# Kernel optimization log

Hardware: AMD Instinct MI355X
Metric: run time of the kernel (lower is better)

Reference implementation:

```python
import math
import jax, jax.numpy as jnp
import numpy as np

H_HEADS = 8
K_MAX = 64
MIN_WINDOW = 1.0
SHARPNESS = 5.0


def rmsnorm(x, w, eps=1e-6):
    x32 = x.astype(jnp.float32)
    var = jnp.mean(x32 * x32, axis=-1, keepdims=True)
    return (w * (x32 * jax.lax.rsqrt(var + eps))).astype(x.dtype)


def setup_inputs() -> dict:
    key = jax.random.key(0)
    ks = jax.random.split(key, 12)
    B, L, C = 1, 4096, 256
    H, K = H_HEADS, K_MAX
    s = 0.02
    return {
        "x": jax.random.normal(ks[0], (B, L, C), jnp.float32),
        "window_w": jax.random.normal(ks[1], (C, H), jnp.float32) * s,
        "window_b": jnp.zeros((H,), jnp.float32),
        "window_gamma": jnp.ones((H,), jnp.float32),
        "offset_w": jax.random.normal(ks[2], (C, H), jnp.float32) * s,
        "offset_b": jnp.zeros((H,), jnp.float32),
        "offset_gamma": jnp.ones((H,), jnp.float32),
        "kernel_w": jax.random.normal(ks[3], (C, H * K), jnp.float32) * s,
        "kernel_b": jnp.zeros((H * K,), jnp.float32),
        "kernel_gamma": jnp.ones((H * K,), jnp.float32),
        "v_w": jax.random.normal(ks[4], (C, C), jnp.float32) * (1.0 / math.sqrt(C)),
        "v_b": jnp.zeros((C,), jnp.float32),
        "out_w": jax.random.normal(ks[5], (C, C), jnp.float32) * s,
    }


def reference(x, window_w, window_b, window_gamma, offset_w, offset_b, offset_gamma,
              kernel_w, kernel_b, kernel_gamma, v_w, v_b, out_w):
    B, L, C = x.shape
    H, K = H_HEADS, K_MAX
    D = C // H
    max_window = min(int(math.sqrt(L)), K)
    half = max_window // 2
    max_offset = int(math.sqrt(L))
    N = 2 * half + 1  # num_offsets

    # per-position learned window sizes, center offsets, kernel weights
    window_raw = jax.nn.sigmoid(rmsnorm(x @ window_w + window_b, window_gamma))
    window_sizes = MIN_WINDOW + window_raw * (max_window - MIN_WINDOW)      # [B,L,H]
    center_offsets = jnp.tanh(rmsnorm(x @ offset_w + offset_b, offset_gamma)) * max_offset  # [B,L,H]
    kernel_weights = jax.nn.silu(rmsnorm(x @ kernel_w + kernel_b, kernel_gamma)).reshape(B, L, H, K)
    v = (x @ v_w + v_b).reshape(B, L, H, D)

    local = jnp.arange(-half, half + 1, dtype=x.dtype)                      # [N]
    positions = jnp.arange(L, dtype=x.dtype).reshape(1, L, 1, 1)
    neighbor = positions + center_offsets[..., None] + local.reshape(1, 1, 1, N)  # [B,L,H,N]
    valid = (neighbor >= 0) & (neighbor < L)
    nclamp = jnp.clip(neighbor, 0, L - 1)

    rel = jnp.abs(local).reshape(1, 1, 1, N) / (window_sizes[..., None] / 2 + 1e-6)
    window_mask = jax.nn.sigmoid(SHARPNESS * (1.0 - rel)) * valid.astype(x.dtype)

    # kernel interpolation by relative distance
    kidx = jnp.clip(rel, 0, 1) * (K - 1)
    i_fl = jnp.clip(kidx.astype(jnp.int32), 0, K - 2)                       # [B,L,H,N]
    i_ce = i_fl + 1
    w_ce = kidx - i_fl.astype(x.dtype)
    k_fl = jnp.take_along_axis(kernel_weights, i_fl, axis=-1)
    k_ce = jnp.take_along_axis(kernel_weights, i_ce, axis=-1)
    kernel_interp = k_fl * (1.0 - w_ce) + k_ce * w_ce

    attn = kernel_interp * window_mask
    attn = attn / (jnp.sum(attn, axis=-1, keepdims=True) + 1e-6)            # [B,L,H,N]

    # bilinear gather of values at fractional neighbor positions
    p_fl = jnp.clip(jnp.floor(nclamp).astype(jnp.int32), 0, L - 1)
    p_ce = jnp.clip(p_fl + 1, 0, L - 1)
    frac = nclamp - p_fl.astype(x.dtype)                                    # [B,L,H,N]

    v_bh = v.transpose(0, 2, 1, 3)                                          # [B,H,L,D]
    idx_f = p_fl.transpose(0, 2, 1, 3).reshape(B, H, L * N)
    idx_c = p_ce.transpose(0, 2, 1, 3).reshape(B, H, L * N)
    v_fl = jnp.take_along_axis(v_bh, idx_f[..., None], axis=2).reshape(B, H, L, N, D)
    v_ce = jnp.take_along_axis(v_bh, idx_c[..., None], axis=2).reshape(B, H, L, N, D)
    frac_bh = frac.transpose(0, 2, 1, 3)[..., None]                         # [B,H,L,N,1]
    v_nb = v_fl * (1.0 - frac_bh) + v_ce * frac_bh                          # [B,H,L,N,D]

    attn_bh = attn.transpose(0, 2, 1, 3)                                    # [B,H,L,N]
    out = jnp.einsum('bhln,bhlnd->bhld', attn_bh, v_nb)                     # [B,H,L,D]
    out = out.transpose(0, 2, 1, 3).reshape(B, L, C)
    return jax.nn.silu(out @ out_w)
```

## Files before the change

### kernel.cpp

```cpp
#include <hip/hip_runtime.h>
#include <math.h>

#define L_SEQ 4096
#define C_DIM 256
#define H_HEADS 8
#define K_MAX 64
#define D_HEAD 32
#define HALF_W 32
#define N_OFF 65
#define HK 512

__device__ __forceinline__ float sigmoidf_(float x) { return 1.0f / (1.0f + expf(-x)); }

__global__ void __launch_bounds__(128, 2)
proj_gemm(const float* __restrict__ A, const float* __restrict__ kw_w,
          const float* __restrict__ vw, const float* __restrict__ kb,
          const float* __restrict__ vb,
          float* __restrict__ kwbuf, float* __restrict__ vbuf) {
    __shared__ float As[16][132];
    __shared__ float Bs[16][68];

    const int tid = threadIdx.x;
    const int tx = tid & 7;
    const int ty = tid >> 3;
    const int l0 = blockIdx.y * 128;
    const int n0 = blockIdx.x * 64;

    const int arow = tid;
    const int bk = tid >> 3;
    const int bn = (tid & 7) * 8;

    const float* Bsrc;
    int ldb, coff;
    if (n0 < 512) { Bsrc = kw_w; ldb = 512; coff = n0; }
    else          { Bsrc = vw;   ldb = 256; coff = n0 - 512; }

    float acc[8][8];
#pragma unroll
    for (int i = 0; i < 8; ++i)
#pragma unroll
        for (int jj = 0; jj < 8; ++jj) acc[i][jj] = 0.0f;

    const float* arow_p = A + (l0 + arow) * C_DIM;
    float4 a0 = *(const float4*)&arow_p[0];
    float4 a1 = *(const float4*)&arow_p[4];
    float4 a2 = *(const float4*)&arow_p[8];
    float4 a3 = *(const float4*)&arow_p[12];
    float4 b0 = *(const float4*)&Bsrc[bk * ldb + coff + bn];
    float4 b1 = *(const float4*)&Bsrc[bk * ldb + coff + bn + 4];

    for (int k0 = 0; k0 < C_DIM; k0 += 16) {
        __syncthreads();
        As[0][arow]  = a0.x; As[1][arow]  = a0.y; As[2][arow]  = a0.z; As[3][arow]  = a0.w;
        As[4][arow]  = a1.x; As[5][arow]  = a1.y; As[6][arow]  = a1.z; As[7][arow]  = a1.w;
        As[8][arow]  = a2.x; As[9][arow]  = a2.y; As[10][arow] = a2.z; As[11][arow] = a2.w;
        As[12][arow] = a3.x; As[13][arow] = a3.y; As[14][arow] = a3.z; As[15][arow] = a3.w;
        *(float4*)&Bs[bk][bn]     = b0;
        *(float4*)&Bs[bk][bn + 4] = b1;
        __syncthreads();
        if (k0 + 16 < C_DIM) {
            a0 = *(const float4*)&arow_p[k0 + 16 + 0];
            a1 = *(const float4*)&arow_p[k0 + 16 + 4];
            a2 = *(const float4*)&arow_p[k0 + 16 + 8];
            a3 = *(const float4*)&arow_p[k0 + 16 + 12];
            b0 = *(const float4*)&Bsrc[(k0 + 16 + bk) * ldb + coff + bn];
            b1 = *(const float4*)&Bsrc[(k0 + 16 + bk) * ldb + coff + bn + 4];
        }
#pragma unroll
        for (int kk = 0; kk < 16; ++kk) {
            const float4 alo = *(const float4*)&As[kk][ty * 8];
            const float4 ahi = *(const float4*)&As[kk][ty * 8 + 4];
            const float4 blo = *(const float4*)&Bs[kk][tx * 8];
            const float4 bhi = *(const float4*)&Bs[kk][tx * 8 + 4];
            const float ar[8] = {alo.x, alo.y, alo.z, alo.w, ahi.x, ahi.y, ahi.z, ahi.w};
            const float br[8] = {blo.x, blo.y, blo.z, blo.w, bhi.x, bhi.y, bhi.z, bhi.w};
#pragma unroll
            for (int i = 0; i < 8; ++i)
#pragma unroll
                for (int jj = 0; jj < 8; ++jj)
                    acc[i][jj] = fmaf(ar[i], br[jj], acc[i][jj]);
        }
    }

    const int g0 = n0 + tx * 8;
    float4 bz0, bz1;
    float* dst;
    int stride, col;
    if (g0 < 512) {
        bz0 = *(const float4*)&kb[g0]; bz1 = *(const float4*)&kb[g0 + 4];
        dst = kwbuf; stride = 512; col = g0;
    } else {
        bz0 = *(const float4*)&vb[g0 - 512]; bz1 = *(const float4*)&vb[g0 - 508];
        dst = vbuf; stride = 256; col = g0 - 512;
    }
#pragma unroll
    for (int i = 0; i < 8; ++i) {
        const int row = l0 + ty * 8 + i;
        float4 o0, o1;
        o0.x = acc[i][0] + bz0.x; o0.y = acc[i][1] + bz0.y;
        o0.z = acc[i][2] + bz0.z; o0.w = acc[i][3] + bz0.w;
        o1.x = acc[i][4] + bz1.x; o1.y = acc[i][5] + bz1.y;
        o1.z = acc[i][6] + bz1.z; o1.w = acc[i][7] + bz1.w;
        *(float4*)&dst[row * stride + col]     = o0;
        *(float4*)&dst[row * stride + col + 4] = o1;
    }
}

__global__ void __launch_bounds__(512, 1)
conv_fused(const float* __restrict__ x,
           const float* __restrict__ ww, const float* __restrict__ wb,
           const float* __restrict__ wg,
           const float* __restrict__ ow, const float* __restrict__ ob,
           const float* __restrict__ og,
           const float* __restrict__ kg,
           const float* __restrict__ kwraw, const float* __restrict__ v,
           float* __restrict__ out) {
    const int l = blockIdx.x;
    const int tid = threadIdx.x;

    __shared__ float red[256];
    __shared__ float rs_s;
    __shared__ float kwrow[HK];
    __shared__ float wsz[H_HEADS], ofs[H_HEADS];
    __shared__ float4 tap[H_HEADS][N_OFF];
    __shared__ float2 warr[H_HEADS][N_OFF + 1];
    __shared__ float inv_denom[H_HEADS];
    __shared__ int okflag;

    float z0 = 0.0f, z1 = 0.0f;
    if (tid < 256) {
        const float* row = kwraw + l * HK;
        z0 = row[tid];
        z1 = row[tid + 256];
        red[tid] = z0 * z0 + z1 * z1;
    } else if (tid < 320) {
        const int lane = tid - 256;
        const float* xr = x + l * C_DIM;
        float accw[H_HEADS], acco[H_HEADS];
#pragma unroll
        for (int h = 0; h < H_HEADS; ++h) { accw[h] = 0.0f; acco[h] = 0.0f; }
#pragma unroll
        for (int i = 0; i < C_DIM / 64; ++i) {
            const int c = lane + i * 64;
            const float xv = xr[c];
            const float* wwc = ww + c * H_HEADS;
            const float* owc = ow + c * H_HEADS;
#pragma unroll
            for (int h = 0; h < H_HEADS; ++h) {
                accw[h] = fmaf(xv, wwc[h], accw[h]);
                acco[h] = fmaf(xv, owc[h], acco[h]);
            }
        }
#pragma unroll
        for (int off = 32; off > 0; off >>= 1) {
#pragma unroll
            for (int h = 0; h < H_HEADS; ++h) {
                accw[h] += __shfl_xor(accw[h], off);
                acco[h] += __shfl_xor(acco[h], off);
            }
        }
        if (lane < H_HEADS) {
            float zw[H_HEADS], zo[H_HEADS];
            float ssw = 0.0f, sso = 0.0f;
#pragma unroll
            for (int h = 0; h < H_HEADS; ++h) {
                zw[h] = accw[h] + wb[h];
                zo[h] = acco[h] + ob[h];
                ssw += zw[h] * zw[h];
                sso += zo[h] * zo[h];
            }
            const float rw = rsqrtf(ssw / (float)H_HEADS + 1e-6f);
            const float ro = rsqrtf(sso / (float)H_HEADS + 1e-6f);
            const float nw = wg[lane] * zw[lane] * rw;
            const float no = og[lane] * zo[lane] * ro;
            wsz[lane] = 1.0f + sigmoidf_(nw) * 63.0f;
            ofs[lane] = tanhf(no) * 64.0f;
        }
    }
    if (tid == 0) okflag = 1;
    __syncthreads();

    if (tid < 128) red[tid] += red[tid + 128];
    __syncthreads();
    if (tid < 64) {
        red[tid] += red[tid + 64];
        if (tid < 32) red[tid] += red[tid + 32];
        if (tid < 16) red[tid] += red[tid + 16];
        if (tid < 8)  red[tid] += red[tid + 8];
        if (tid < 4)  red[tid] += red[tid + 4];
        if (tid < 2)  red[tid] += red[tid + 2];
        if (tid < 1) {
            red[0] += red[1];
            rs_s = rsqrtf(red[0] / (float)HK + 1e-6f);
        }
    }
    __syncthreads();
    if (tid < 256) {
        const float rs = rs_s;
        const float n0v = kg[tid] * z0 * rs;
        const float n1v = kg[tid + 256] * z1 * rs;
        kwrow[tid]       = n0v * sigmoidf_(n0v);
        kwrow[tid + 256] = n1v * sigmoidf_(n1v);
    }
    __syncthreads();

    for (int t = tid; t < H_HEADS * N_OFF; t += 512) {
        const int h = t / N_OFF;
        const int n = t - h * N_OFF;
        const float ws  = wsz[h];
        const float off = ofs[h];
        const float local = (float)(n - HALF_W);
        const float neighbor = (float)l + off + local;
        const bool valid = (neighbor >= 0.0f) && (neighbor < (float)L_SEQ);
        const float nc = fminf(fmaxf(neighbor, 0.0f), (float)(L_SEQ - 1));

        const float rel = fabsf(local) / (ws * 0.5f + 1e-6f);
        const float mask = sigmoidf_(5.0f * (1.0f - rel)) * (valid ? 1.0f : 0.0f);

        const float kidx = fminf(rel, 1.0f) * (float)(K_MAX - 1);
        int ifl = (int)kidx;
        ifl = min(ifl, K_MAX - 2);
        const float wce = kidx - (float)ifl;
        const float kf = kwrow[h * K_MAX + ifl];
        const float kc = kwrow[h * K_MAX + ifl + 1];
        const float attnv = (kf * (1.0f - wce) + kc * wce) * mask;

        int p = (int)floorf(nc);
        p = min(max(p, 0), L_SEQ - 1);
        const int pc = min(p + 1, L_SEQ - 1);
        const float fr = nc - (float)p;

        float4 tv;
        tv.x = attnv;
        tv.y = fr;
        tv.z = __int_as_float(p * C_DIM + h * D_HEAD);
        tv.w = __int_as_float(pc * C_DIM + h * D_HEAD);
        tap[h][n] = tv;
    }
    __syncthreads();

    for (int t = tid; t < H_HEADS * (N_OFF + 1); t += 512) {
        const int h = t / (N_OFF + 1);
        const int m = t - h * (N_OFF + 1);
        float w, rowf;
        if (m == 0) {
            const float4 cur = tap[h][0];
            w = cur.x * (1.0f - cur.y);
            rowf = cur.z;
        } else {
            const float4 prev = tap[h][m - 1];
            const float wc = prev.x * prev.y;
            if (m < N_OFF) {
                const float4 cur = tap[h][m];
                w = cur.x * (1.0f - cur.y) + wc;
                rowf = cur.z;
                if (wc != 0.0f && __float_as_int(prev.w) != __float_as_int(cur.z))
                    okflag = 0;
            } else {
                w = wc;
                rowf = prev.w;
            }
        }
        warr[h][m] = make_float2(w, rowf);
    }

    if (tid < H_HEADS) {
        float s = 0.0f;
        for (int n = 0; n < N_OFF; ++n) s += tap[tid][n].x;
        inv_denom[tid] = 1.0f / (s + 1e-6f);
    }
    __syncthreads();

    const int h = tid >> 6;
    const int lane = tid & 63;
    const int half = lane >> 5;
    const int d = lane & 31;
    float acc = 0.0f;
    if (okflag) {
#pragma unroll 3
        for (int it = 0; it < (N_OFF + 1) / 2; ++it) {
            const float2 t2 = warr[h][2 * it + half];
            acc = fmaf(t2.x, v[__float_as_int(t2.y) + d], acc);
        }
    } else {
#pragma unroll 3
        for (int it = 0; it < 33; ++it) {
            const int n = 2 * it + half;
            if (n < N_OFF) {
                const float4 t4 = tap[h][n];
                const float vf = v[__float_as_int(t4.z) + d];
                const float vc = v[__float_as_int(t4.w) + d];
                acc = fmaf(t4.x, fmaf(t4.y, vc - vf, vf), acc);
            }
        }
    }
    acc += __shfl_xor(acc, 32);
    if (half == 0) out[l * C_DIM + h * D_HEAD + d] = acc * inv_denom[h];
}

__global__ void __launch_bounds__(256, 4)
out_gemm(const float* __restrict__ A, const float* __restrict__ W,
         float* __restrict__ out) {
    __shared__ float As[16][68];
    __shared__ float Bs[16][68];

    const int tid = threadIdx.x;
    const int tx = tid & 15;
    const int ty = tid >> 4;
    const int l0 = blockIdx.y * 64;
    const int n0 = blockIdx.x * 64;

    const int am = tid >> 2;
    const int ak = (tid & 3) * 4;
    const int bk = tid >> 4;
    const int bn = (tid & 15) * 4;

    float acc[4][4];
#pragma unroll
    for (int i = 0; i < 4; ++i)
#pragma unroll
        for (int jj = 0; jj < 4; ++jj) acc[i][jj] = 0.0f;

    float4 av = *(const float4*)&A[(l0 + am) * C_DIM + ak];
    float4 bv = *(const float4*)&W[bk * C_DIM + n0 + bn];

    for (int k0 = 0; k0 < C_DIM; k0 += 16) {
        __syncthreads();
        As[ak + 0][am] = av.x;
        As[ak + 1][am] = av.y;
        As[ak + 2][am] = av.z;
        As[ak + 3][am] = av.w;
        *(float4*)&Bs[bk][bn] = bv;
        __syncthreads();
        if (k0 + 16 < C_DIM) {
            av = *(const float4*)&A[(l0 + am) * C_DIM + (k0 + 16) + ak];
            bv = *(const float4*)&W[(k0 + 16 + bk) * C_DIM + n0 + bn];
        }
#pragma unroll
        for (int kk = 0; kk < 16; ++kk) {
            const float4 a4 = *(const float4*)&As[kk][ty * 4];
            const float4 b4 = *(const float4*)&Bs[kk][tx * 4];
            const float ar[4] = {a4.x, a4.y, a4.z, a4.w};
            const float br[4] = {b4.x, b4.y, b4.z, b4.w};
#pragma unroll
            for (int i = 0; i < 4; ++i)
#pragma unroll
                for (int jj = 0; jj < 4; ++jj)
                    acc[i][jj] = fmaf(ar[i], br[jj], acc[i][jj]);
        }
    }

    const int g0 = n0 + tx * 4;
#pragma unroll
    for (int i = 0; i < 4; ++i) {
        const int row = l0 + ty * 4 + i;
        float4 o;
        o.x = acc[i][0] * sigmoidf_(acc[i][0]);
        o.y = acc[i][1] * sigmoidf_(acc[i][1]);
        o.z = acc[i][2] * sigmoidf_(acc[i][2]);
        o.w = acc[i][3] * sigmoidf_(acc[i][3]);
        *(float4*)&out[row * C_DIM + g0] = o;
    }
}

extern "C" void kernel_launch(void* const* d_in, const int* in_sizes, int n_in,
                              void* d_out, int out_size, void* d_ws, size_t ws_size,
                              hipStream_t stream) {
    const float* x    = (const float*)d_in[0];
    const float* ww   = (const float*)d_in[1];
    const float* wb   = (const float*)d_in[2];
    const float* wg   = (const float*)d_in[3];
    const float* ow   = (const float*)d_in[4];
    const float* ob   = (const float*)d_in[5];
    const float* og   = (const float*)d_in[6];
    const float* kw_w = (const float*)d_in[7];
    const float* kb   = (const float*)d_in[8];
    const float* kg   = (const float*)d_in[9];
    const float* vw   = (const float*)d_in[10];
    const float* vb   = (const float*)d_in[11];
    const float* outw = (const float*)d_in[12];
    float* y = (float*)d_out;

    float* ws_f    = (float*)d_ws;
    float* kwbuf   = ws_f;
    float* vbuf    = kwbuf + L_SEQ * HK;
    float* convbuf = vbuf + L_SEQ * C_DIM;

    proj_gemm<<<dim3(12, L_SEQ / 128), 128, 0, stream>>>(x, kw_w, vw, kb, vb, kwbuf, vbuf);
    conv_fused<<<L_SEQ, 512, 0, stream>>>(x, ww, wb, wg, ow, ob, og, kg, kwbuf, vbuf, convbuf);
    out_gemm<<<dim3(C_DIM / 64, L_SEQ / 64), 256, 0, stream>>>(convbuf, outw, y);
}
```

Before: 184.5 us.

## Halve conv_fused block to 256 threads with per-thread full-tap loop

```diff
diff --git a/kernel.cpp b/kernel.cpp
--- a/kernel.cpp
+++ b/kernel.cpp
@@ -106,7 +106,7 @@
     }
 }
 
-__global__ void __launch_bounds__(512, 1)
+__global__ void __launch_bounds__(256, 2)
 conv_fused(const float* __restrict__ x,
            const float* __restrict__ ww, const float* __restrict__ wb,
            const float* __restrict__ wg,
@@ -127,14 +127,19 @@
     __shared__ float inv_denom[H_HEADS];
     __shared__ int okflag;
 
-    float z0 = 0.0f, z1 = 0.0f;
-    if (tid < 256) {
+    if (tid == 0) okflag = 1;
+
+    float z0a = 0, z0b = 0, z1a = 0, z1b = 0;
+    if (tid >= 128) {
+        const int j0 = tid - 128;
+        const int j1 = tid;
         const float* row = kwraw + l * HK;
-        z0 = row[tid];
-        z1 = row[tid + 256];
-        red[tid] = z0 * z0 + z1 * z1;
-    } else if (tid < 320) {
-        const int lane = tid - 256;
+        z0a = row[j0]; z0b = row[j0 + 256];
+        z1a = row[j1]; z1b = row[j1 + 256];
+        red[j0] = z0a * z0a + z0b * z0b;
+        red[j1] = z1a * z1a + z1b * z1b;
+    } else if (tid < 64) {
+        const int lane = tid;
         const float* xr = x + l * C_DIM;
         float accw[H_HEADS], acco[H_HEADS];
 #pragma unroll
@@ -177,34 +182,30 @@
             ofs[lane] = tanhf(no) * 64.0f;
         }
     }
-    if (tid == 0) okflag = 1;
     __syncthreads();
 
     if (tid < 128) red[tid] += red[tid + 128];
     __syncthreads();
     if (tid < 64) {
-        red[tid] += red[tid + 64];
-        if (tid < 32) red[tid] += red[tid + 32];
-        if (tid < 16) red[tid] += red[tid + 16];
-        if (tid < 8)  red[tid] += red[tid + 8];
-        if (tid < 4)  red[tid] += red[tid + 4];
-        if (tid < 2)  red[tid] += red[tid + 2];
-        if (tid < 1) {
-            red[0] += red[1];
-            rs_s = rsqrtf(red[0] / (float)HK + 1e-6f);
-        }
-    }
-    __syncthreads();
-    if (tid < 256) {
+        float s = red[tid] + red[tid + 64];
+#pragma unroll
+        for (int off = 32; off > 0; off >>= 1) s += __shfl_xor(s, off);
+        if (tid == 0) rs_s = rsqrtf(s / (float)HK + 1e-6f);
+    }
+    __syncthreads();
+
+    if (tid >= 128) {
         const float rs = rs_s;
-        const float n0v = kg[tid] * z0 * rs;
-        const float n1v = kg[tid + 256] * z1 * rs;
-        kwrow[tid]       = n0v * sigmoidf_(n0v);
-        kwrow[tid + 256] = n1v * sigmoidf_(n1v);
-    }
-    __syncthreads();
-
-    for (int t = tid; t < H_HEADS * N_OFF; t += 512) {
+        const int j0 = tid - 128, j1 = tid;
+        float n;
+        n = kg[j0]       * z0a * rs; kwrow[j0]       = n * sigmoidf_(n);
+        n = kg[j0 + 256] * z0b * rs; kwrow[j0 + 256] = n * sigmoidf_(n);
+        n = kg[j1]       * z1a * rs; kwrow[j1]       = n * sigmoidf_(n);
+        n = kg[j1 + 256] * z1b * rs; kwrow[j1 + 256] = n * sigmoidf_(n);
+    }
+    __syncthreads();
+
+    for (int t = tid; t < H_HEADS * N_OFF; t += 256) {
         const int h = t / N_OFF;
         const int n = t - h * N_OFF;
         const float ws  = wsz[h];
@@ -239,63 +240,59 @@
     }
     __syncthreads();
 
-    for (int t = tid; t < H_HEADS * (N_OFF + 1); t += 512) {
-        const int h = t / (N_OFF + 1);
-        const int m = t - h * (N_OFF + 1);
-        float w, rowf;
-        if (m == 0) {
-            const float4 cur = tap[h][0];
-            w = cur.x * (1.0f - cur.y);
-            rowf = cur.z;
-        } else {
-            const float4 prev = tap[h][m - 1];
-            const float wc = prev.x * prev.y;
-            if (m < N_OFF) {
-                const float4 cur = tap[h][m];
-                w = cur.x * (1.0f - cur.y) + wc;
-                rowf = cur.z;
-                if (wc != 0.0f && __float_as_int(prev.w) != __float_as_int(cur.z))
-                    okflag = 0;
-            } else {
-                w = wc;
-                rowf = prev.w;
-            }
-        }
-        warr[h][m] = make_float2(w, rowf);
-    }
-
-    if (tid < H_HEADS) {
+    if (tid < 8) {
         float s = 0.0f;
         for (int n = 0; n < N_OFF; ++n) s += tap[tid][n].x;
         inv_denom[tid] = 1.0f / (s + 1e-6f);
-    }
-    __syncthreads();
-
-    const int h = tid >> 6;
-    const int lane = tid & 63;
-    const int half = lane >> 5;
-    const int d = lane & 31;
+    } else {
+        for (int t = tid - 8; t < H_HEADS * (N_OFF + 1); t += 248) {
+            const int h = t / (N_OFF + 1);
+            const int m = t - h * (N_OFF + 1);
+            float w, rowf;
+            if (m == 0) {
+                const float4 cur = tap[h][0];
+                w = cur.x * (1.0f - cur.y);
+                rowf = cur.z;
+            } else {
+                const float4 prev = tap[h][m - 1];
+                const float wc = prev.x * prev.y;
+                if (m < N_OFF) {
+                    const float4 cur = tap[h][m];
+                    w = cur.x * (1.0f - cur.y) + wc;
+                    rowf = cur.z;
+                    if (wc != 0.0f && __float_as_int(prev.w) != __float_as_int(cur.z))
+                        okflag = 0;
+                } else {
+                    w = wc;
+                    rowf = prev.w;
+                }
+            }
+            warr[h][m] = make_float2(w, rowf);
+        }
+    }
+    __syncthreads();
+
+    const int h = tid >> 5;
+    const int d = tid & 31;
     float acc = 0.0f;
     if (okflag) {
-#pragma unroll 3
-        for (int it = 0; it < (N_OFF + 1) / 2; ++it) {
-            const float2 t2 = warr[h][2 * it + half];
+#pragma unroll 6
+        for (int m = 0; m < N_OFF + 1; ++m) {
+            const float2 t2 = warr[h][m];
             acc = fmaf(t2.x, v[__float_as_int(t2.y) + d], acc);
         }
     } else {
-#pragma unroll 3
-        for (int it = 0; it < 33; ++it) {
-            const int n = 2 * it + half;
-            if (n < N_OFF) {
-                const float4 t4 = tap[h][n];
-                const float vf = v[__float_as_int(t4.z) + d];
-                const float vc = v[__float_as_int(t4.w) + d];
-                acc = fmaf(t4.x, fmaf(t4.y, vc - vf, vf), acc);
-            }
-        }
-    }
-    acc += __shfl_xor(acc, 32);
-    if (half == 0) out[l * C_DIM + h * D_HEAD + d] = acc * inv_denom[h];
+#pragma unroll 5
+        for (int n = 0; n < N_OFF; ++n) {
+            const float4 t4 = tap[h][n];
+            const int bf = __float_as_int(t4.z);
+            const int bc = __float_as_int(t4.w);
+            const float vf = v[bf + d];
+            const float vc = v[bc + d];
+            acc = fmaf(t4.x, fmaf(t4.y, vc - vf, vf), acc);
+        }
+    }
+    out[l * C_DIM + h * D_HEAD + d] = acc * inv_denom[h];
 }
 
 __global__ void __launch_bounds__(256, 4)
@@ -387,6 +384,6 @@
     float* convbuf = vbuf + L_SEQ * C_DIM;
 
     proj_gemm<<<dim3(12, L_SEQ / 128), 128, 0, stream>>>(x, kw_w, vw, kb, vb, kwbuf, vbuf);
-    conv_fused<<<L_SEQ, 512, 0, stream>>>(x, ww, wb, wg, ow, ob, og, kg, kwbuf, vbuf, convbuf);
+    conv_fused<<<L_SEQ, 256, 0, stream>>>(x, ww, wb, wg, ow, ob, og, kg, kwbuf, vbuf, convbuf);
     out_gemm<<<dim3(C_DIM / 64, L_SEQ / 64), 256, 0, stream>>>(convbuf, outw, y);
 }
```

Result: faster. 163.0 us (-11.7%).
